# Kernel tuning notes

Measured on AMD Instinct MI355X. Metric: run time of the kernel, lower is better.

## Reference

```python
import itertools
import jax, jax.numpy as jnp
import numpy as np

N_QUBITS = 8
N_LAYERS = 2
BATCH = 8192
INPUT_DIM = 3072
NUM_CLASSES = 10

_In = np.eye(2, dtype=np.complex64)
_Xn = np.array([[0, 1], [1, 0]], dtype=np.complex64)
_Yn = np.array([[0, -1j], [1j, 0]], dtype=np.complex64)
_Zn = np.array([[1, 0], [0, -1]], dtype=np.complex64)
_P = {"I": _In, "X": _Xn, "Y": _Yn, "Z": _Zn}
_XX = jnp.asarray(np.kron(_Xn, _Xn))
_YY = jnp.asarray(np.kron(_Yn, _Yn))
_ZZ = jnp.asarray(np.kron(_Zn, _Zn))
_I4 = jnp.eye(4, dtype=jnp.complex64)
# 2-qubit Pauli words in PennyLane ArbitraryUnitary order: IX, IY, IZ, XI, ..., ZZ
_WORDS = jnp.asarray(np.stack([np.kron(_P[a], _P[b]) for a, b in itertools.product("IXYZ", repeat=2)][1:]))


def apply_gate(state, U, wires):
    """Apply a 2^k x 2^k gate U to the given wires of a (2,)*n statevector."""
    n = state.ndim
    k = len(wires)
    U = U.reshape((2,) * (2 * k)).astype(state.dtype)
    state = jnp.tensordot(U, state, axes=(list(range(k, 2 * k)), list(wires)))
    rest = [a for a in range(n) if a not in wires]
    perm = [0] * n
    for i, a in enumerate(wires):
        perm[a] = i
    for j, a in enumerate(rest):
        perm[a] = k + j
    return jnp.transpose(state, perm)


def u3_mat(t, p, d):
    ct, st = jnp.cos(t / 2).astype(jnp.complex64), jnp.sin(t / 2).astype(jnp.complex64)
    r0 = jnp.stack([ct, -jnp.exp(1j * d) * st])
    r1 = jnp.stack([jnp.exp(1j * p) * st, jnp.exp(1j * (p + d)) * ct])
    return jnp.stack([r0, r1])


def ry_mat(t):
    c, s = jnp.cos(t / 2), jnp.sin(t / 2)
    return jnp.stack([jnp.stack([c, -s]), jnp.stack([s, c])]).astype(jnp.complex64)


def ising_mat(phi, pauli2):
    # exp(-i phi/2 P) for two-qubit Pauli word P (P^2 = I)
    return jnp.cos(phi / 2) * _I4 - 1j * jnp.sin(phi / 2) * pauli2


def circuit(conv_w, pool_w, last_w, feats):
    state = jnp.zeros((2,) * N_QUBITS, jnp.complex64).at[(0,) * N_QUBITS].set(1.0)
    # AngleEmbedding with RY rotations
    for w in range(N_QUBITS):
        state = apply_gate(state, ry_mat(feats[w]), (w,))
    wires = list(range(N_QUBITS))
    for layer in range(N_LAYERS):
        cw = conv_w[layer]
        nw = len(wires)
        for p in (0, 1):
            for idx in range(nw - 1):
                if idx % 2 == p:
                    a, b = wires[idx], wires[idx + 1]
                    state = apply_gate(state, u3_mat(cw[idx, 0], cw[idx, 1], cw[idx, 2]), (a,))
                    state = apply_gate(state, u3_mat(cw[idx + 1, 3], cw[idx + 1, 4], cw[idx + 1, 5]), (b,))
                    state = apply_gate(state, ising_mat(cw[idx, 6], _ZZ), (a, b))
                    state = apply_gate(state, ising_mat(cw[idx, 7], _YY), (a, b))
                    state = apply_gate(state, ising_mat(cw[idx, 8], _XX), (a, b))
                    state = apply_gate(state, u3_mat(cw[idx, 9], cw[idx, 10], cw[idx, 11]), (a,))
                    state = apply_gate(state, u3_mat(cw[idx + 1, 12], cw[idx + 1, 13], cw[idx + 1, 14]), (b,))
        # Pooling: mid-circuit measure + conditional U3 == (deferred measurement)
        pw = pool_w[layer]
        for idx in range(1, nw, 2):
            u = u3_mat(pw[idx // 2, 0], pw[idx // 2, 1], pw[idx // 2, 2])
            cu = jnp.zeros((4, 4), jnp.complex64).at[0, 0].set(1.0).at[1, 1].set(1.0).at[2:, 2:].set(u)
            state = apply_gate(state, cu, (wires[idx], wires[idx - 1]))
        wires = wires[::2]
    # ArbitraryUnitary on remaining 2 wires: product of 15 PauliRot gates
    for k in range(15):
        mat = jnp.cos(last_w[k] / 2) * _I4 - 1j * jnp.sin(last_w[k] / 2) * _WORDS[k]
        state = apply_gate(state, mat, tuple(wires))
    probs = state.real ** 2 + state.imag ** 2
    z = jnp.sum(probs, axis=tuple(range(1, N_QUBITS)))  # (2,)
    return z[0] - z[1]


def setup_inputs() -> dict:
    key = jax.random.key(0)
    ks = jax.random.split(key, 8)
    return {
        "x": jax.random.normal(ks[0], (BATCH, INPUT_DIM), jnp.float32),
        "fc_w": jax.random.normal(ks[1], (N_QUBITS, INPUT_DIM), jnp.float32) * 0.02,
        "fc_b": jnp.zeros((N_QUBITS,), jnp.float32),
        "conv_params": jax.random.normal(ks[2], (N_LAYERS, N_QUBITS, 15), jnp.float32),
        "pool_params": jax.random.normal(ks[3], (N_LAYERS, N_QUBITS // 2, 3), jnp.float32),
        "last_params": jax.random.normal(ks[4], (15,), jnp.float32),
        "out_w": jax.random.normal(ks[5], (NUM_CLASSES, 1), jnp.float32),
        "out_b": jnp.zeros((NUM_CLASSES,), jnp.float32),
    }


def reference(x, fc_w, fc_b, conv_params, pool_params, last_params, out_w, out_b):
    feats = jnp.tanh(x.reshape(x.shape[0], -1) @ fc_w.T + fc_b)  # (B, n_qubits)
    qvals = jax.vmap(lambda f: circuit(conv_params, pool_params, last_params, f))(feats)
    logits = qvals[:, None].astype(x.dtype) @ out_w.T + out_b  # (B, num_classes)
    return logits
```

## Files before the change

kernel.cpp:

```cpp
#include <hip/hip_runtime.h>
#include <math.h>

__constant__ int G_ORD[17] = {0,1,2,3,4,5,6, 10,11,12,13, 7,8,9, 14,15, 16};
__constant__ int G_WA[17]  = {0,2,4,6,1,3,5, 1,3,5,7, 0,4,2, 2,6, 0};
__constant__ int G_WB[17]  = {1,3,5,7,2,4,6, 0,2,4,6, 2,6,4, 0,4, 4};
__constant__ int CDESC[10][3] = {{0,0,1},{0,2,3},{0,4,5},{0,6,7},{0,1,2},{0,3,4},{0,5,6},
                                 {1,0,1},{1,2,3},{1,1,2}};
__constant__ int PDESC[6][2] = {{0,0},{0,1},{0,2},{0,3},{1,0},{1,1}};
__constant__ float2 PMAT[4][4] = {
  {{1.f,0.f},{0.f,0.f},{0.f,0.f},{1.f,0.f}},
  {{0.f,0.f},{1.f,0.f},{1.f,0.f},{0.f,0.f}},
  {{0.f,0.f},{0.f,-1.f},{0.f,1.f},{0.f,0.f}},
  {{1.f,0.f},{0.f,0.f},{0.f,0.f},{-1.f,0.f}}};

__device__ __forceinline__ float2 cmul(float2 a, float2 b){
  return make_float2(a.x*b.x - a.y*b.y, a.x*b.y + a.y*b.x);
}
__device__ __forceinline__ float2 cadd(float2 a, float2 b){
  return make_float2(a.x+b.x, a.y+b.y);
}

__device__ void u3m(float t, float p, float d, float2* u){
  float ct = cosf(0.5f*t), st = sinf(0.5f*t);
  u[0] = make_float2(ct, 0.f);
  u[1] = make_float2(-cosf(d)*st, -sinf(d)*st);
  u[2] = make_float2(cosf(p)*st,  sinf(p)*st);
  u[3] = make_float2(cosf(p+d)*ct, sinf(p+d)*ct);
}

__device__ void kron2(const float2* A, const float2* B, float2* M){
  #pragma unroll
  for (int ia=0; ia<2; ia++)
    #pragma unroll
    for (int ib=0; ib<2; ib++)
      #pragma unroll
      for (int ja=0; ja<2; ja++)
        #pragma unroll
        for (int jb=0; jb<2; jb++)
          M[(ia*2+ib)*4 + (ja*2+jb)] = cmul(A[ia*2+ja], B[ib*2+jb]);
}

__device__ void mul44(const float2* A, const float2* B, float2* C){
  #pragma unroll
  for (int r=0;r<4;r++)
    #pragma unroll
    for (int c=0;c<4;c++){
      float2 s = make_float2(0.f,0.f);
      #pragma unroll
      for (int k=0;k<4;k++) s = cadd(s, cmul(A[r*4+k], B[k*4+c]));
      C[r*4+c] = s;
    }
}

__device__ void rotword(float phi, int qa, int qb, float2* R){
  float ch = cosf(0.5f*phi), sh = sinf(0.5f*phi);
  float2 W[16];
  kron2(PMAT[qa], PMAT[qb], W);
  #pragma unroll
  for (int i=0;i<16;i++) R[i] = make_float2(sh*W[i].y, -sh*W[i].x);
  #pragma unroll
  for (int d=0;d<4;d++) R[d*4+d].x += ch;
}

__global__ __launch_bounds__(64) void build_u_kernel(
    const float* __restrict__ conv, const float* __restrict__ pool,
    const float* __restrict__ last, float2* __restrict__ U){
  __shared__ float2 gl[17][16];
  __shared__ float2 st[256];
  int t = threadIdx.x, col = blockIdx.x;
  {
    float2 M[16], T[16], R[16];
    if (t < 10){
      int layer = CDESC[t][0], ra = CDESC[t][1], rb = CDESC[t][2];
      const float* cw = conv + layer*120;
      int bA = ra*15, bB = rb*15;
      float2 A1[4], B1[4], A2[4], B2[4], K[16];
      u3m(cw[bA+0], cw[bA+1], cw[bA+2], A1);
      u3m(cw[bB+3], cw[bB+4], cw[bB+5], B1);
      kron2(A1, B1, M);
      rotword(cw[bA+6], 3, 3, R); mul44(R, M, T);
      rotword(cw[bA+7], 2, 2, R); mul44(R, T, M);
      rotword(cw[bA+8], 1, 1, R); mul44(R, M, T);
      u3m(cw[bA+9],  cw[bA+10], cw[bA+11], A2);
      u3m(cw[bB+12], cw[bB+13], cw[bB+14], B2);
      kron2(A2, B2, K); mul44(K, T, M);
    } else if (t < 16){
      int layer = PDESC[t-10][0], h = PDESC[t-10][1];
      const float* pw = pool + layer*12 + h*3;
      float2 u[4];
      u3m(pw[0], pw[1], pw[2], u);
      #pragma unroll
      for (int i=0;i<16;i++) M[i] = make_float2(0.f,0.f);
      M[0]  = make_float2(1.f,0.f);
      M[5]  = make_float2(1.f,0.f);
      M[10] = u[0]; M[11] = u[1]; M[14] = u[2]; M[15] = u[3];
    } else if (t == 16){
      #pragma unroll
      for (int i=0;i<16;i++) M[i] = make_float2((i%5==0)?1.f:0.f, 0.f);
      for (int k=0;k<15;k++){
        int w = k+1;
        rotword(last[k], w>>2, w&3, R);
        mul44(R, M, T);
        #pragma unroll
        for (int i=0;i<16;i++) M[i] = T[i];
      }
    }
    if (t < 17){
      #pragma unroll
      for (int i=0;i<16;i++) gl[t][i] = M[i];
    }
  }
  #pragma unroll
  for (int k=t; k<256; k+=64) st[k] = make_float2(k==col ? 1.f : 0.f, 0.f);
  __syncthreads();
  for (int g=0; g<17; g++){
    int slot = G_ORD[g];
    float2 m[16];
    #pragma unroll
    for (int i=0;i<16;i++) m[i] = gl[slot][i];
    int pa = 7 - G_WA[g], pb = 7 - G_WB[g];
    int plo = pa < pb ? pa : pb, phi_ = pa < pb ? pb : pa;
    int mm = t;
    int t1   = ((mm >> plo) << (plo+1)) | (mm & ((1<<plo)-1));
    int base = ((t1 >> phi_) << (phi_+1)) | (t1 & ((1<<phi_)-1));
    int ba = 1<<pa, bb = 1<<pb;
    int i0 = base, i1 = base|bb, i2 = base|ba, i3 = base|ba|bb;
    float2 s0 = st[i0], s1 = st[i1], s2 = st[i2], s3 = st[i3];
    float2 n0 = cadd(cadd(cmul(m[0], s0), cmul(m[1], s1)), cadd(cmul(m[2], s2), cmul(m[3], s3)));
    float2 n1 = cadd(cadd(cmul(m[4], s0), cmul(m[5], s1)), cadd(cmul(m[6], s2), cmul(m[7], s3)));
    float2 n2 = cadd(cadd(cmul(m[8], s0), cmul(m[9], s1)), cadd(cmul(m[10],s2), cmul(m[11],s3)));
    float2 n3 = cadd(cadd(cmul(m[12],s0), cmul(m[13],s1)), cadd(cmul(m[14],s2), cmul(m[15],s3)));
    st[i0] = n0; st[i1] = n1; st[i2] = n2; st[i3] = n3;
    __syncthreads();
  }
  #pragma unroll
  for (int k=t; k<256; k+=64) U[k*256 + col] = st[k];
}

__global__ __launch_bounds__(256) void build_a_kernel(
    const float2* __restrict__ U, float* __restrict__ A){
  int j = threadIdx.x, i0 = blockIdx.x*2;
  float a0=0.f, a1=0.f;
  #pragma unroll 8
  for (int k=0; k<256; k++){
    float2 uj = U[k*256 + j];
    float2 u0 = U[k*256 + i0+0];
    float2 u1 = U[k*256 + i0+1];
    float sgn = (k < 128) ? 1.f : -1.f;
    a0 += sgn*(u0.x*uj.x + u0.y*uj.y);
    a1 += sgn*(u1.x*uj.x + u1.y*uj.y);
  }
  A[(i0+0)*256 + j] = a0;
  A[(i0+1)*256 + j] = a1;
}

__global__ __launch_bounds__(256) void main_kernel(
    const float* __restrict__ x, const float* __restrict__ fcw,
    const float* __restrict__ fcb, const float* __restrict__ Ag,
    const float* __restrict__ outw, const float* __restrict__ outb,
    float* __restrict__ out){
  __shared__ float lds[12288];
  __shared__ float flds[128];
  float* red = lds;
  float* As  = lds;
  float* ps  = lds + 8192;
  int t = threadIdx.x, lane = t & 63, wv = t >> 6, jb = lane;
  int r0 = blockIdx.x * 16;
  {
    int rw = r0 + wv*4;
    const float4* x4 = (const float4*)x;
    const float4* w4 = (const float4*)fcw;
    float acc[4][8];
    #pragma unroll
    for (int r=0;r<4;r++)
      #pragma unroll
      for (int o=0;o<8;o++) acc[r][o] = 0.f;
    #pragma unroll 2
    for (int p=0; p<12; p++){
      float4 wf[8];
      #pragma unroll
      for (int o=0;o<8;o++) wf[o] = w4[o*768 + p*64 + lane];
      #pragma unroll
      for (int r=0;r<4;r++){
        float4 xv = x4[(size_t)(rw+r)*768 + p*64 + lane];
        #pragma unroll
        for (int o=0;o<8;o++){
          acc[r][o] += xv.x*wf[o].x + xv.y*wf[o].y + xv.z*wf[o].z + xv.w*wf[o].w;
        }
      }
    }
    #pragma unroll
    for (int r=0;r<4;r++)
      #pragma unroll
      for (int o=0;o<8;o++)
        red[((wv*4+r)*8 + o)*68 + lane] = acc[r][o];
  }
  __syncthreads();
  if (t < 128){
    const float4* rp = (const float4*)(red + t*68);
    float4 s4 = make_float4(0.f,0.f,0.f,0.f);
    #pragma unroll
    for (int i=0;i<16;i++){
      float4 v = rp[i];
      s4.x += v.x; s4.y += v.y; s4.z += v.z; s4.w += v.w;
    }
    flds[t] = tanhf(s4.x + s4.y + s4.z + s4.w + fcb[t & 7]);
  }
  __syncthreads();
  float psi_local[16];
  {
    int row = t >> 4, i1 = t & 15;
    const float* f = flds + row*8;
    float c[8], s[8];
    #pragma unroll
    for (int w=0; w<8; w++){
      float a = 0.5f*f[w];
      __sincosf(a, &s[w], &c[w]);
    }
    float Hv = (i1&8 ? s[0]:c[0]) * (i1&4 ? s[1]:c[1])
             * (i1&2 ? s[2]:c[2]) * (i1&1 ? s[3]:c[3]);
    float l2[2], l4[4], l8[8], L[16];
    l2[0]=c[4]; l2[1]=s[4];
    #pragma unroll
    for (int a=0;a<2;a++){ l4[a*2]=l2[a]*c[5]; l4[a*2+1]=l2[a]*s[5]; }
    #pragma unroll
    for (int a=0;a<4;a++){ l8[a*2]=l4[a]*c[6]; l8[a*2+1]=l4[a]*s[6]; }
    #pragma unroll
    for (int a=0;a<8;a++){ L[a*2]=l8[a]*c[7]; L[a*2+1]=l8[a]*s[7]; }
    #pragma unroll
    for (int j=0;j<16;j++) psi_local[j] = Hv*L[j];
  }
  __syncthreads();
  {
    int row = t >> 4, i1 = t & 15;
    float4* dst = (float4*)(ps + row*256 + i1*16);
    #pragma unroll
    for (int qd=0; qd<4; qd++)
      dst[qd] = make_float4(psi_local[qd*4+0], psi_local[qd*4+1],
                            psi_local[qd*4+2], psi_local[qd*4+3]);
  }
  const float4* As4 = (const float4*)As;
  const float4* ps4 = (const float4*)ps;
  const float4* Ag4 = (const float4*)Ag;
  float4 acc4[4];
  #pragma unroll
  for (int r=0;r<4;r++) acc4[r] = make_float4(0.f,0.f,0.f,0.f);
  for (int chunk=0; chunk<8; chunk++){
    __syncthreads();
    #pragma unroll
    for (int pass=0; pass<8; pass++){
      int kk = pass*4 + wv;
      *(float4*)(As + kk*256 + jb*4) = Ag4[(chunk*32 + kk)*64 + jb];
    }
    __syncthreads();
    #pragma unroll
    for (int kq=0; kq<8; kq++){
      float4 av0 = As4[(kq*4+0)*64 + jb];
      float4 av1 = As4[(kq*4+1)*64 + jb];
      float4 av2 = As4[(kq*4+2)*64 + jb];
      float4 av3 = As4[(kq*4+3)*64 + jb];
      #pragma unroll
      for (int r=0; r<4; r++){
        float4 pv = ps4[(wv*4+r)*64 + chunk*8 + kq];
        acc4[r].x += pv.x*av0.x + pv.y*av1.x + pv.z*av2.x + pv.w*av3.x;
        acc4[r].y += pv.x*av0.y + pv.y*av1.y + pv.z*av2.y + pv.w*av3.y;
        acc4[r].z += pv.x*av0.z + pv.y*av1.z + pv.z*av2.z + pv.w*av3.z;
        acc4[r].w += pv.x*av0.w + pv.y*av1.w + pv.z*av2.w + pv.w*av3.w;
      }
    }
  }
  float p[4];
  #pragma unroll
  for (int r=0; r<4; r++){
    float4 psv = ps4[(wv*4+r)*64 + jb];
    float pr = acc4[r].x*psv.x + acc4[r].y*psv.y + acc4[r].z*psv.z + acc4[r].w*psv.w;
    #pragma unroll
    for (int m=1; m<64; m<<=1) pr += __shfl_xor(pr, m, 64);
    p[r] = pr;
  }
  if (jb < 40){
    int ridx = jb / 10, c = jb - ridx*10;
    float q = (ridx==0) ? p[0] : (ridx==1) ? p[1] : (ridx==2) ? p[2] : p[3];
    out[(r0 + wv*4 + ridx)*10 + c] = q*outw[c] + outb[c];
  }
}

extern "C" void kernel_launch(void* const* d_in, const int* in_sizes, int n_in,
                              void* d_out, int out_size, void* d_ws, size_t ws_size,
                              hipStream_t stream) {
  const float* x    = (const float*)d_in[0];
  const float* fcw  = (const float*)d_in[1];
  const float* fcb  = (const float*)d_in[2];
  const float* conv = (const float*)d_in[3];
  const float* pool = (const float*)d_in[4];
  const float* last = (const float*)d_in[5];
  const float* outw = (const float*)d_in[6];
  const float* outb = (const float*)d_in[7];
  float* out = (float*)d_out;

  float* ws = (float*)d_ws;
  float2* U  = (float2*)ws;
  float*  Am = ws + 131072;

  build_u_kernel<<<256, 64, 0, stream>>>(conv, pool, last, U);
  build_a_kernel<<<128, 256, 0, stream>>>(U, Am);
  main_kernel<<<512, 256, 0, stream>>>(x, fcw, fcb, Am, outw, outb, out);
}
```

Measured before the change: 246.9 us.

## Build gate matrices in a dedicated parallel kernel and shrink main-kernel row tiles

```diff
diff --git a/kernel.cpp b/kernel.cpp
--- a/kernel.cpp
+++ b/kernel.cpp
@@ -28,88 +28,94 @@
   u[3] = make_float2(cosf(p+d)*ct, sinf(p+d)*ct);
 }
 
-__device__ void kron2(const float2* A, const float2* B, float2* M){
-  #pragma unroll
-  for (int ia=0; ia<2; ia++)
-    #pragma unroll
-    for (int ib=0; ib<2; ib++)
-      #pragma unroll
-      for (int ja=0; ja<2; ja++)
-        #pragma unroll
-        for (int jb=0; jb<2; jb++)
-          M[(ia*2+ib)*4 + (ja*2+jb)] = cmul(A[ia*2+ja], B[ib*2+jb]);
-}
-
-__device__ void mul44(const float2* A, const float2* B, float2* C){
-  #pragma unroll
-  for (int r=0;r<4;r++)
-    #pragma unroll
-    for (int c=0;c<4;c++){
-      float2 s = make_float2(0.f,0.f);
-      #pragma unroll
-      for (int k=0;k<4;k++) s = cadd(s, cmul(A[r*4+k], B[k*4+c]));
-      C[r*4+c] = s;
-    }
-}
-
-__device__ void rotword(float phi, int qa, int qb, float2* R){
-  float ch = cosf(0.5f*phi), sh = sinf(0.5f*phi);
-  float2 W[16];
-  kron2(PMAT[qa], PMAT[qb], W);
-  #pragma unroll
-  for (int i=0;i<16;i++) R[i] = make_float2(sh*W[i].y, -sh*W[i].x);
-  #pragma unroll
-  for (int d=0;d<4;d++) R[d*4+d].x += ch;
+__global__ __launch_bounds__(320) void build_gates_kernel(
+    const float* __restrict__ conv, const float* __restrict__ pool,
+    const float* __restrict__ last, float2* __restrict__ G){
+  __shared__ float2 gm[2][17][16];
+  int t = threadIdx.x;
+  int g = t >> 4, e = t & 15, r = e >> 2, c = e & 3;
+  float2 A1[4], B1[4], A2[4], B2[4];
+  int nsteps = 0;
+  if (g < 10){
+    int layer = CDESC[g][0], ra = CDESC[g][1], rb = CDESC[g][2];
+    const float* cw = conv + layer*120;
+    int bA = ra*15, bB = rb*15;
+    u3m(cw[bA+0],  cw[bA+1],  cw[bA+2],  A1);
+    u3m(cw[bB+3],  cw[bB+4],  cw[bB+5],  B1);
+    u3m(cw[bA+9],  cw[bA+10], cw[bA+11], A2);
+    u3m(cw[bB+12], cw[bB+13], cw[bB+14], B2);
+    nsteps = 5;
+  } else if (g < 16){
+    nsteps = 1;
+  } else if (g == 16){
+    nsteps = 16;
+  }
+  for (int s = 0; s < 16; s++){
+    if (g < 17 && s < nsteps){
+      float2 T = make_float2(0.f, 0.f);
+      if (g < 10){
+        if (s == 0){
+          T = cmul(A1[(r>>1)*2 + (c>>1)], B1[(r&1)*2 + (c&1)]);
+        } else if (s <= 3){
+          int layer = CDESC[g][0], ra = CDESC[g][1];
+          float phi = conv[layer*120 + ra*15 + 5 + s];
+          int q_ = 4 - s;
+          float ch = cosf(0.5f*phi), sh = sinf(0.5f*phi);
+          #pragma unroll
+          for (int k=0;k<4;k++){
+            float2 w = cmul(PMAT[q_][(r>>1)*2 + (k>>1)], PMAT[q_][(r&1)*2 + (k&1)]);
+            float2 rk = make_float2(sh*w.y, -sh*w.x);
+            if (k == r) rk.x += ch;
+            T = cadd(T, cmul(rk, gm[s&1][g][k*4 + c]));
+          }
+        } else {
+          #pragma unroll
+          for (int k=0;k<4;k++){
+            float2 k2 = cmul(A2[(r>>1)*2 + (k>>1)], B2[(r&1)*2 + (k&1)]);
+            T = cadd(T, cmul(k2, gm[s&1][g][k*4 + c]));
+          }
+        }
+      } else if (g < 16){
+        int layer = PDESC[g-10][0], h = PDESC[g-10][1];
+        const float* pw = pool + layer*12 + h*3;
+        float2 u[4];
+        u3m(pw[0], pw[1], pw[2], u);
+        if (e == 0 || e == 5) T = make_float2(1.f, 0.f);
+        else if (e == 10) T = u[0];
+        else if (e == 11) T = u[1];
+        else if (e == 14) T = u[2];
+        else if (e == 15) T = u[3];
+      } else {
+        if (s == 0){
+          T = make_float2((r==c)?1.f:0.f, 0.f);
+        } else {
+          int w_ = s;
+          int qa = w_ >> 2, qb = w_ & 3;
+          float phi = last[s-1];
+          float ch = cosf(0.5f*phi), sh = sinf(0.5f*phi);
+          #pragma unroll
+          for (int k=0;k<4;k++){
+            float2 w = cmul(PMAT[qa][(r>>1)*2 + (k>>1)], PMAT[qb][(r&1)*2 + (k&1)]);
+            float2 rk = make_float2(sh*w.y, -sh*w.x);
+            if (k == r) rk.x += ch;
+            T = cadd(T, cmul(rk, gm[s&1][16][k*4 + c]));
+          }
+        }
+      }
+      gm[(s+1)&1][g][e] = T;
+      if (s == nsteps-1) G[g*16 + e] = T;
+    }
+    __syncthreads();
+  }
 }
 
 __global__ __launch_bounds__(64) void build_u_kernel(
-    const float* __restrict__ conv, const float* __restrict__ pool,
-    const float* __restrict__ last, float2* __restrict__ U){
+    const float2* __restrict__ G, float2* __restrict__ U){
   __shared__ float2 gl[17][16];
   __shared__ float2 st[256];
   int t = threadIdx.x, col = blockIdx.x;
-  {
-    float2 M[16], T[16], R[16];
-    if (t < 10){
-      int layer = CDESC[t][0], ra = CDESC[t][1], rb = CDESC[t][2];
-      const float* cw = conv + layer*120;
-      int bA = ra*15, bB = rb*15;
-      float2 A1[4], B1[4], A2[4], B2[4], K[16];
-      u3m(cw[bA+0], cw[bA+1], cw[bA+2], A1);
-      u3m(cw[bB+3], cw[bB+4], cw[bB+5], B1);
-      kron2(A1, B1, M);
-      rotword(cw[bA+6], 3, 3, R); mul44(R, M, T);
-      rotword(cw[bA+7], 2, 2, R); mul44(R, T, M);
-      rotword(cw[bA+8], 1, 1, R); mul44(R, M, T);
-      u3m(cw[bA+9],  cw[bA+10], cw[bA+11], A2);
-      u3m(cw[bB+12], cw[bB+13], cw[bB+14], B2);
-      kron2(A2, B2, K); mul44(K, T, M);
-    } else if (t < 16){
-      int layer = PDESC[t-10][0], h = PDESC[t-10][1];
-      const float* pw = pool + layer*12 + h*3;
-      float2 u[4];
-      u3m(pw[0], pw[1], pw[2], u);
-      #pragma unroll
-      for (int i=0;i<16;i++) M[i] = make_float2(0.f,0.f);
-      M[0]  = make_float2(1.f,0.f);
-      M[5]  = make_float2(1.f,0.f);
-      M[10] = u[0]; M[11] = u[1]; M[14] = u[2]; M[15] = u[3];
-    } else if (t == 16){
-      #pragma unroll
-      for (int i=0;i<16;i++) M[i] = make_float2((i%5==0)?1.f:0.f, 0.f);
-      for (int k=0;k<15;k++){
-        int w = k+1;
-        rotword(last[k], w>>2, w&3, R);
-        mul44(R, M, T);
-        #pragma unroll
-        for (int i=0;i<16;i++) M[i] = T[i];
-      }
-    }
-    if (t < 17){
-      #pragma unroll
-      for (int i=0;i<16;i++) gl[t][i] = M[i];
-    }
-  }
+  float2* glf = (float2*)gl;
+  for (int k=t; k<272; k+=64) glf[k] = G[k];
   #pragma unroll
   for (int k=t; k<256; k+=64) st[k] = make_float2(k==col ? 1.f : 0.f, 0.f);
   __syncthreads();
@@ -139,40 +145,37 @@
 
 __global__ __launch_bounds__(256) void build_a_kernel(
     const float2* __restrict__ U, float* __restrict__ A){
-  int j = threadIdx.x, i0 = blockIdx.x*2;
-  float a0=0.f, a1=0.f;
+  int j = threadIdx.x, i = blockIdx.x;
+  float a = 0.f;
   #pragma unroll 8
   for (int k=0; k<256; k++){
     float2 uj = U[k*256 + j];
-    float2 u0 = U[k*256 + i0+0];
-    float2 u1 = U[k*256 + i0+1];
+    float2 ui = U[k*256 + i];
     float sgn = (k < 128) ? 1.f : -1.f;
-    a0 += sgn*(u0.x*uj.x + u0.y*uj.y);
-    a1 += sgn*(u1.x*uj.x + u1.y*uj.y);
-  }
-  A[(i0+0)*256 + j] = a0;
-  A[(i0+1)*256 + j] = a1;
-}
-
-__global__ __launch_bounds__(256) void main_kernel(
+    a += sgn*(ui.x*uj.x + ui.y*uj.y);
+  }
+  A[i*256 + j] = a;
+}
+
+__global__ __launch_bounds__(256, 4) void main_kernel(
     const float* __restrict__ x, const float* __restrict__ fcw,
     const float* __restrict__ fcb, const float* __restrict__ Ag,
     const float* __restrict__ outw, const float* __restrict__ outb,
     float* __restrict__ out){
-  __shared__ float lds[12288];
-  __shared__ float flds[128];
-  float* red = lds;
-  float* As  = lds;
-  float* ps  = lds + 8192;
+  __shared__ float lds[10240];
+  float* red  = lds;
+  float* As   = lds;
+  float* ps   = lds + 8192;
+  float* flds = lds + 8192;
   int t = threadIdx.x, lane = t & 63, wv = t >> 6, jb = lane;
-  int r0 = blockIdx.x * 16;
+  int r0 = blockIdx.x * 8;
   {
-    int rw = r0 + wv*4;
+    int rw = r0 + wv*2;
     const float4* x4 = (const float4*)x;
     const float4* w4 = (const float4*)fcw;
-    float acc[4][8];
-    #pragma unroll
-    for (int r=0;r<4;r++)
+    float acc[2][8];
+    #pragma unroll
+    for (int r=0;r<2;r++)
       #pragma unroll
       for (int o=0;o<8;o++) acc[r][o] = 0.f;
     #pragma unroll 2
@@ -181,7 +184,7 @@
       #pragma unroll
       for (int o=0;o<8;o++) wf[o] = w4[o*768 + p*64 + lane];
       #pragma unroll
-      for (int r=0;r<4;r++){
+      for (int r=0;r<2;r++){
         float4 xv = x4[(size_t)(rw+r)*768 + p*64 + lane];
         #pragma unroll
         for (int o=0;o<8;o++){
@@ -190,13 +193,13 @@
       }
     }
     #pragma unroll
-    for (int r=0;r<4;r++)
+    for (int r=0;r<2;r++)
       #pragma unroll
       for (int o=0;o<8;o++)
-        red[((wv*4+r)*8 + o)*68 + lane] = acc[r][o];
+        red[((wv*2+r)*8 + o)*68 + lane] = acc[r][o];
   }
   __syncthreads();
-  if (t < 128){
+  if (t < 64){
     const float4* rp = (const float4*)(red + t*68);
     float4 s4 = make_float4(0.f,0.f,0.f,0.f);
     #pragma unroll
@@ -208,30 +211,32 @@
   }
   __syncthreads();
   float psi_local[16];
-  {
+  if (t < 128){
     int row = t >> 4, i1 = t & 15;
-    const float* f = flds + row*8;
-    float c[8], s[8];
+    float fv[8];
+    #pragma unroll
+    for (int w=0; w<8; w++) fv[w] = flds[row*8 + w];
+    float cc[8], ss[8];
     #pragma unroll
     for (int w=0; w<8; w++){
-      float a = 0.5f*f[w];
-      __sincosf(a, &s[w], &c[w]);
-    }
-    float Hv = (i1&8 ? s[0]:c[0]) * (i1&4 ? s[1]:c[1])
-             * (i1&2 ? s[2]:c[2]) * (i1&1 ? s[3]:c[3]);
+      float a = 0.5f*fv[w];
+      __sincosf(a, &ss[w], &cc[w]);
+    }
+    float Hv = (i1&8 ? ss[0]:cc[0]) * (i1&4 ? ss[1]:cc[1])
+             * (i1&2 ? ss[2]:cc[2]) * (i1&1 ? ss[3]:cc[3]);
     float l2[2], l4[4], l8[8], L[16];
-    l2[0]=c[4]; l2[1]=s[4];
-    #pragma unroll
-    for (int a=0;a<2;a++){ l4[a*2]=l2[a]*c[5]; l4[a*2+1]=l2[a]*s[5]; }
-    #pragma unroll
-    for (int a=0;a<4;a++){ l8[a*2]=l4[a]*c[6]; l8[a*2+1]=l4[a]*s[6]; }
-    #pragma unroll
-    for (int a=0;a<8;a++){ L[a*2]=l8[a]*c[7]; L[a*2+1]=l8[a]*s[7]; }
+    l2[0]=cc[4]; l2[1]=ss[4];
+    #pragma unroll
+    for (int a=0;a<2;a++){ l4[a*2]=l2[a]*cc[5]; l4[a*2+1]=l2[a]*ss[5]; }
+    #pragma unroll
+    for (int a=0;a<4;a++){ l8[a*2]=l4[a]*cc[6]; l8[a*2+1]=l4[a]*ss[6]; }
+    #pragma unroll
+    for (int a=0;a<8;a++){ L[a*2]=l8[a]*cc[7]; L[a*2+1]=l8[a]*ss[7]; }
     #pragma unroll
     for (int j=0;j<16;j++) psi_local[j] = Hv*L[j];
   }
   __syncthreads();
-  {
+  if (t < 128){
     int row = t >> 4, i1 = t & 15;
     float4* dst = (float4*)(ps + row*256 + i1*16);
     #pragma unroll
@@ -242,9 +247,9 @@
   const float4* As4 = (const float4*)As;
   const float4* ps4 = (const float4*)ps;
   const float4* Ag4 = (const float4*)Ag;
-  float4 acc4[4];
+  float4 acc4[2];
   #pragma unroll
-  for (int r=0;r<4;r++) acc4[r] = make_float4(0.f,0.f,0.f,0.f);
+  for (int r=0;r<2;r++) acc4[r] = make_float4(0.f,0.f,0.f,0.f);
   for (int chunk=0; chunk<8; chunk++){
     __syncthreads();
     #pragma unroll
@@ -260,8 +265,8 @@
       float4 av2 = As4[(kq*4+2)*64 + jb];
       float4 av3 = As4[(kq*4+3)*64 + jb];
       #pragma unroll
-      for (int r=0; r<4; r++){
-        float4 pv = ps4[(wv*4+r)*64 + chunk*8 + kq];
+      for (int r=0; r<2; r++){
+        float4 pv = ps4[(wv*2+r)*64 + chunk*8 + kq];
         acc4[r].x += pv.x*av0.x + pv.y*av1.x + pv.z*av2.x + pv.w*av3.x;
         acc4[r].y += pv.x*av0.y + pv.y*av1.y + pv.z*av2.y + pv.w*av3.y;
         acc4[r].z += pv.x*av0.z + pv.y*av1.z + pv.z*av2.z + pv.w*av3.z;
@@ -269,19 +274,19 @@
       }
     }
   }
-  float p[4];
+  float p[2];
   #pragma unroll
-  for (int r=0; r<4; r++){
-    float4 psv = ps4[(wv*4+r)*64 + jb];
+  for (int r=0; r<2; r++){
+    float4 psv = ps4[(wv*2+r)*64 + jb];
     float pr = acc4[r].x*psv.x + acc4[r].y*psv.y + acc4[r].z*psv.z + acc4[r].w*psv.w;
     #pragma unroll
     for (int m=1; m<64; m<<=1) pr += __shfl_xor(pr, m, 64);
     p[r] = pr;
   }
-  if (jb < 40){
+  if (jb < 20){
     int ridx = jb / 10, c = jb - ridx*10;
-    float q = (ridx==0) ? p[0] : (ridx==1) ? p[1] : (ridx==2) ? p[2] : p[3];
-    out[(r0 + wv*4 + ridx)*10 + c] = q*outw[c] + outb[c];
+    float q = (ridx==0) ? p[0] : p[1];
+    out[(r0 + wv*2 + ridx)*10 + c] = q*outw[c] + outb[c];
   }
 }
 
@@ -301,8 +306,10 @@
   float* ws = (float*)d_ws;
   float2* U  = (float2*)ws;
   float*  Am = ws + 131072;
-
-  build_u_kernel<<<256, 64, 0, stream>>>(conv, pool, last, U);
-  build_a_kernel<<<128, 256, 0, stream>>>(U, Am);
-  main_kernel<<<512, 256, 0, stream>>>(x, fcw, fcb, Am, outw, outb, out);
-}
+  float2* G  = (float2*)(ws + 131072);
+
+  build_gates_kernel<<<1, 320, 0, stream>>>(conv, pool, last, G);
+  build_u_kernel<<<256, 64, 0, stream>>>(G, U);
+  build_a_kernel<<<256, 256, 0, stream>>>(U, Am);
+  main_kernel<<<1024, 256, 0, stream>>>(x, fcw, fcb, Am, outw, outb, out);
+}
```

Result: slower. 256.8 us (+4.0%).
